# Performance work log

Measured on AMD Instinct MI355X. Metric: run time of the kernel, lower is better.

## Reference

```python
import jax, jax.numpy as jnp
import numpy as np

B, N, D, DH = 8, 2048, 1024, 64

def setup_inputs() -> dict:
    key = jax.random.key(0)
    ks = jax.random.split(key, 4)
    s = 1.0 / np.sqrt(D)
    return {
        "x": jax.random.normal(ks[0], (B, N, D), dtype=jnp.float32),
        "Wq": jax.random.normal(ks[1], (D, DH), dtype=jnp.float32) * s,
        "bq": jnp.zeros((DH,), dtype=jnp.float32),
        "Wk": jax.random.normal(ks[2], (D, DH), dtype=jnp.float32) * s,
        "bk": jnp.zeros((DH,), dtype=jnp.float32),
        "Wv": jax.random.normal(ks[3], (D, DH), dtype=jnp.float32) * s,
        "bv": jnp.zeros((DH,), dtype=jnp.float32),
    }

def reference(x, Wq, bq, Wk, bk, Wv, bv):
    # Projections: [B,N,DH]
    Q = x @ Wq + bq
    K = x @ Wk + bk
    V = x @ Wv + bv
    sqrt_dh = jnp.sqrt(jnp.asarray(DH, dtype=x.dtype))
    # scores[b,i,j] = Q_i . K_j  (original materializes [B,N,N,DH]; GEMM is equivalent math)
    att = jnp.einsum("bid,bjd->bij", Q, K) / sqrt_dh
    # NOTE: original softmaxes over dim=1 (the query/i axis), not the usual j axis.
    att = jax.nn.softmax(att, axis=1)
    # Dropout is identity in eval mode.
    return jnp.einsum("bij,bjd->bid", att, V)
```

## Files before the change

kernel.cpp:

```cpp
#include <hip/hip_runtime.h>
#include <math.h>

#define Bn  8
#define Nn  2048
#define Dn  1024
#define DHn 64
#define PAD 72

typedef __attribute__((ext_vector_type(8))) short bf16x8;
typedef __attribute__((ext_vector_type(4))) float f32x4;

static __device__ inline short f2bf(float f) {
    unsigned u = __builtin_bit_cast(unsigned, f);
    u += 0x7FFFu + ((u >> 16) & 1u);
    return (short)(u >> 16);
}
static __device__ inline bf16x8 pack8(float4 a, float4 b) {
    bf16x8 v;
    v[0] = f2bf(a.x); v[1] = f2bf(a.y); v[2] = f2bf(a.z); v[3] = f2bf(a.w);
    v[4] = f2bf(b.x); v[5] = f2bf(b.y); v[6] = f2bf(b.z); v[7] = f2bf(b.w);
    return v;
}

__global__ __launch_bounds__(128) void wt_kernel(
    const float* __restrict__ Wq, const float* __restrict__ Wk,
    const float* __restrict__ Wv, short* __restrict__ Wtf)
{
    const int nt = blockIdx.x / 16, kt = blockIdx.x % 16;
    const int t = threadIdx.x;
    const int half = t >> 6, l = t & 63;
    const int c = l & 15, quad = l >> 4;
    const int mat = nt >> 2, cm = (nt & 3) * 16 + c;
    const float* Wm = (mat == 0) ? Wq : (mat == 1 ? Wk : Wv);
    short* o = &Wtf[((((size_t)nt * 16 + kt) * 2 + half) * 64 + l) * 8];
#pragma unroll
    for (int e = 0; e < 8; ++e) {
        const int k = kt * 64 + half * 32 + quad * 8 + e;
        o[e] = f2bf(Wm[(size_t)k * DHn + cm]);
    }
}

__global__ __launch_bounds__(256) void qkv_kernel(
    const float* __restrict__ x, const short* __restrict__ Wtf,
    const float* __restrict__ bq, const float* __restrict__ bk,
    const float* __restrict__ bv,
    short* __restrict__ Qb, short* __restrict__ Kb, short* __restrict__ Vt)
{
    __shared__ __attribute__((aligned(16))) short xs[2][32][PAD];

    const int t = threadIdx.x;
    const int w = t >> 6, l = t & 63;
    const int c = l & 15, quad = l >> 4;
    const int ibase = blockIdx.x * 32;
    const int r0 = t >> 3, kc = t & 7;

    const float* xrow = &x[(size_t)(ibase + r0) * Dn + kc * 8];

    {
        const float4 a = ((const float4*)xrow)[0];
        const float4 b = ((const float4*)xrow)[1];
        *(bf16x8*)&xs[0][r0][kc * 8] = pack8(a, b);
    }

    f32x4 acc[2][3];
#pragma unroll
    for (int mt = 0; mt < 2; ++mt)
#pragma unroll
        for (int nt = 0; nt < 3; ++nt) acc[mt][nt] = (f32x4){0.f, 0.f, 0.f, 0.f};

    __syncthreads();

    for (int kt = 0; kt < 16; ++kt) {
        const int cur = kt & 1;
        float4 pa, pb;
        if (kt < 15) {
            pa = ((const float4*)(xrow + (kt + 1) * 64))[0];
            pb = ((const float4*)(xrow + (kt + 1) * 64))[1];
        }
#pragma unroll
        for (int h = 0; h < 2; ++h) {
            const bf16x8 af0 = *(const bf16x8*)&xs[cur][c][h * 32 + quad * 8];
            const bf16x8 af1 = *(const bf16x8*)&xs[cur][16 + c][h * 32 + quad * 8];
#pragma unroll
            for (int nt = 0; nt < 3; ++nt) {
                const int ntg = w * 3 + nt;
                const bf16x8 bf = *(const bf16x8*)&Wtf[((((size_t)ntg * 16 + kt) * 2 + h) * 64 + l) * 8];
                acc[0][nt] = __builtin_amdgcn_mfma_f32_16x16x32_bf16(af0, bf, acc[0][nt], 0, 0, 0);
                acc[1][nt] = __builtin_amdgcn_mfma_f32_16x16x32_bf16(af1, bf, acc[1][nt], 0, 0, 0);
            }
        }
        if (kt < 15) *(bf16x8*)&xs[1 - cur][r0][kc * 8] = pack8(pa, pb);
        __syncthreads();
    }

#pragma unroll
    for (int nt = 0; nt < 3; ++nt) {
        const int col = w * 48 + nt * 16 + c;
        const int mat = col >> 6, cm = col & 63;
        const float bias = (mat == 0 ? bq : (mat == 1 ? bk : bv))[cm];
#pragma unroll
        for (int mt = 0; mt < 2; ++mt) {
            if (mat == 2) {
                const int row = ibase + mt * 16 + quad * 4;
                const int b = row >> 11, i = row & (Nn - 1);
                ushort4 o;
                o.x = (unsigned short)f2bf(acc[mt][nt][0] + bias);
                o.y = (unsigned short)f2bf(acc[mt][nt][1] + bias);
                o.z = (unsigned short)f2bf(acc[mt][nt][2] + bias);
                o.w = (unsigned short)f2bf(acc[mt][nt][3] + bias);
                *(ushort4*)&Vt[((size_t)b * DHn + cm) * Nn + i] = o;
            } else {
                const float s = (mat == 1) ? 0.125f : 1.0f;
                short* Out = (mat == 0) ? Qb : Kb;
#pragma unroll
                for (int r = 0; r < 4; ++r)
                    Out[(size_t)(ibase + mt * 16 + quad * 4 + r) * DHn + cm] =
                        f2bf((acc[mt][nt][r] + bias) * s);
            }
        }
    }
}

__global__ __launch_bounds__(256) void colsum_kernel(
    const short* __restrict__ Qb, const short* __restrict__ Kb,
    float* __restrict__ lpart)
{
    __shared__ __attribute__((aligned(16))) short Qw[4][2][16][PAD];
    __shared__ float red[16][64];

    const int t = threadIdx.x;
    const int w = t >> 6, l = t & 63;
    const int c = l & 15, quad = l >> 4;
    const int bid = blockIdx.x;
    const int b = bid >> 7, rem = bid & 127, jt = rem >> 2, s = rem & 3;
    const int jbase = jt * 64;
    const int srow = l >> 2, scol = (l & 3) * 16;

    bf16x8 kb[4][2];
#pragma unroll
    for (int nt = 0; nt < 4; ++nt)
#pragma unroll
        for (int kk = 0; kk < 2; ++kk)
            kb[nt][kk] = *(const bf16x8*)&Kb[((size_t)b * Nn + jbase + nt * 16 + c) * DHn
                                             + kk * 32 + quad * 8];

    const short* qbase = &Qb[((size_t)b * Nn + s * 512 + w * 16 + srow) * DHn + scol];

    *(bf16x8*)&Qw[w][0][srow][scol]     = *(const bf16x8*)qbase;
    *(bf16x8*)&Qw[w][0][srow][scol + 8] = *(const bf16x8*)(qbase + 8);

    float lsum[4] = {0.f, 0.f, 0.f, 0.f};

    for (int ch = 0; ch < 8; ++ch) {
        const int cur = ch & 1;
        bf16x8 p0, p1;
        if (ch < 7) {
            const short* pq = qbase + (size_t)(ch + 1) * 64 * DHn;
            p0 = *(const bf16x8*)pq; p1 = *(const bf16x8*)(pq + 8);
        }
        const bf16x8 aq0 = *(const bf16x8*)&Qw[w][cur][c][quad * 8];
        const bf16x8 aq1 = *(const bf16x8*)&Qw[w][cur][c][32 + quad * 8];
#pragma unroll
        for (int nt = 0; nt < 4; ++nt) {
            f32x4 sv = (f32x4){0.f, 0.f, 0.f, 0.f};
            sv = __builtin_amdgcn_mfma_f32_16x16x32_bf16(aq0, kb[nt][0], sv, 0, 0, 0);
            sv = __builtin_amdgcn_mfma_f32_16x16x32_bf16(aq1, kb[nt][1], sv, 0, 0, 0);
            lsum[nt] += __expf(sv[0]) + __expf(sv[1]) + __expf(sv[2]) + __expf(sv[3]);
        }
        if (ch < 7) {
            *(bf16x8*)&Qw[w][1 - cur][srow][scol]     = p0;
            *(bf16x8*)&Qw[w][1 - cur][srow][scol + 8] = p1;
        }
    }

#pragma unroll
    for (int nt = 0; nt < 4; ++nt) red[w * 4 + quad][nt * 16 + c] = lsum[nt];
    __syncthreads();
    if (t < 64) {
        float sum = 0.f;
#pragma unroll
        for (int r = 0; r < 16; ++r) sum += red[r][t];
        lpart[((size_t)s * Bn + b) * Nn + jbase + t] = sum;
    }
}

__global__ __launch_bounds__(256) void attnout_kernel(
    const short* __restrict__ Qb, const short* __restrict__ Kb,
    const short* __restrict__ Vt, const float* __restrict__ lpart,
    float* __restrict__ outp)
{
    __shared__ __attribute__((aligned(16))) short Ks[2][64][PAD];
    __shared__ __attribute__((aligned(16))) short Vs[2][64][PAD];
    __shared__ __attribute__((aligned(16))) short Ps[4][16][PAD];
    __shared__ float rls[2][64];

    const int t = threadIdx.x;
    const int w = t >> 6, lane = t & 63;
    const int c = lane & 15, quad = lane >> 4;
    const int bid = blockIdx.x;
    const int b = bid >> 7, rem = bid & 127, it = rem >> 2, s = rem & 3;
    const int ibase = it * 64;
    const int r0 = t >> 2, cc = (t & 3) * 16;

    const size_t qrow = (size_t)b * Nn + ibase + w * 16 + c;
    const bf16x8 aq0 = *(const bf16x8*)&Qb[qrow * DHn + quad * 8];
    const bf16x8 aq1 = *(const bf16x8*)&Qb[qrow * DHn + 32 + quad * 8];

    const short* kbase = &Kb[((size_t)b * Nn + s * 512 + r0) * DHn + cc];
    const short* vbase = &Vt[((size_t)b * DHn + r0) * Nn + s * 512 + cc];

    *(bf16x8*)&Ks[0][r0][cc]     = *(const bf16x8*)kbase;
    *(bf16x8*)&Ks[0][r0][cc + 8] = *(const bf16x8*)(kbase + 8);
    *(bf16x8*)&Vs[0][r0][cc]     = *(const bf16x8*)vbase;
    *(bf16x8*)&Vs[0][r0][cc + 8] = *(const bf16x8*)(vbase + 8);
    if (t < 64) {
        const size_t lj = (size_t)b * Nn + s * 512 + t;
        rls[0][t] = 1.0f / (lpart[lj] + lpart[(size_t)Bn * Nn + lj]
                          + lpart[2 * (size_t)Bn * Nn + lj] + lpart[3 * (size_t)Bn * Nn + lj]);
    }

    f32x4 acc[4];
#pragma unroll
    for (int dn = 0; dn < 4; ++dn) acc[dn] = (f32x4){0.f, 0.f, 0.f, 0.f};
    __syncthreads();

    for (int jt2 = 0; jt2 < 8; ++jt2) {
        const int cur = jt2 & 1;
        bf16x8 pk0, pk1, pv0, pv1; float nrl;
        if (jt2 < 7) {
            const short* pk = kbase + (size_t)(jt2 + 1) * 64 * DHn;
            pk0 = *(const bf16x8*)pk; pk1 = *(const bf16x8*)(pk + 8);
            const short* pv = vbase + (jt2 + 1) * 64;
            pv0 = *(const bf16x8*)pv; pv1 = *(const bf16x8*)(pv + 8);
            if (t < 64) {
                const size_t lj = (size_t)b * Nn + s * 512 + (jt2 + 1) * 64 + t;
                nrl = 1.0f / (lpart[lj] + lpart[(size_t)Bn * Nn + lj]
                            + lpart[2 * (size_t)Bn * Nn + lj] + lpart[3 * (size_t)Bn * Nn + lj]);
            }
        }

#pragma unroll
        for (int nt = 0; nt < 4; ++nt) {
            const bf16x8 kb0 = *(const bf16x8*)&Ks[cur][nt * 16 + c][quad * 8];
            const bf16x8 kb1 = *(const bf16x8*)&Ks[cur][nt * 16 + c][32 + quad * 8];
            f32x4 sv = (f32x4){0.f, 0.f, 0.f, 0.f};
            sv = __builtin_amdgcn_mfma_f32_16x16x32_bf16(aq0, kb0, sv, 0, 0, 0);
            sv = __builtin_amdgcn_mfma_f32_16x16x32_bf16(aq1, kb1, sv, 0, 0, 0);
            const float rl = rls[cur][nt * 16 + c];
#pragma unroll
            for (int r = 0; r < 4; ++r)
                Ps[w][quad * 4 + r][nt * 16 + c] = f2bf(__expf(sv[r]) * rl);
        }
        const bf16x8 ap0 = *(const bf16x8*)&Ps[w][c][quad * 8];
        const bf16x8 ap1 = *(const bf16x8*)&Ps[w][c][32 + quad * 8];
#pragma unroll
        for (int dn = 0; dn < 4; ++dn) {
            const bf16x8 vb0 = *(const bf16x8*)&Vs[cur][dn * 16 + c][quad * 8];
            const bf16x8 vb1 = *(const bf16x8*)&Vs[cur][dn * 16 + c][32 + quad * 8];
            acc[dn] = __builtin_amdgcn_mfma_f32_16x16x32_bf16(ap0, vb0, acc[dn], 0, 0, 0);
            acc[dn] = __builtin_amdgcn_mfma_f32_16x16x32_bf16(ap1, vb1, acc[dn], 0, 0, 0);
        }

        if (jt2 < 7) {
            *(bf16x8*)&Ks[1 - cur][r0][cc]     = pk0;
            *(bf16x8*)&Ks[1 - cur][r0][cc + 8] = pk1;
            *(bf16x8*)&Vs[1 - cur][r0][cc]     = pv0;
            *(bf16x8*)&Vs[1 - cur][r0][cc + 8] = pv1;
            if (t < 64) rls[1 - cur][t] = nrl;
        }
        __syncthreads();
    }

    float* op = outp + (size_t)s * (Bn * Nn * DHn) + ((size_t)b * Nn + ibase) * DHn;
#pragma unroll
    for (int dn = 0; dn < 4; ++dn)
#pragma unroll
        for (int r = 0; r < 4; ++r)
            op[(w * 16 + quad * 4 + r) * DHn + dn * 16 + c] = acc[dn][r];
}

__global__ __launch_bounds__(256) void outreduce_kernel(
    const float* __restrict__ outp, float* __restrict__ out)
{
    const int id = blockIdx.x * 256 + threadIdx.x;
    const float4* p = (const float4*)outp;
    const float4 a = p[id];
    const float4 b = p[id + 262144];
    const float4 c = p[id + 2 * 262144];
    const float4 d = p[id + 3 * 262144];
    float4 r;
    r.x = a.x + b.x + c.x + d.x;
    r.y = a.y + b.y + c.y + d.y;
    r.z = a.z + b.z + c.z + d.z;
    r.w = a.w + b.w + c.w + d.w;
    ((float4*)out)[id] = r;
}

extern "C" void kernel_launch(void* const* d_in, const int* in_sizes, int n_in,
                              void* d_out, int out_size, void* d_ws, size_t ws_size,
                              hipStream_t stream)
{
    const float* x  = (const float*)d_in[0];
    const float* Wq = (const float*)d_in[1];
    const float* bq = (const float*)d_in[2];
    const float* Wk = (const float*)d_in[3];
    const float* bk = (const float*)d_in[4];
    const float* Wv = (const float*)d_in[5];
    const float* bv = (const float*)d_in[6];
    float* out = (float*)d_out;

    char* ws = (char*)d_ws;
    short* Qb    = (short*)(ws);
    short* Kb    = (short*)(ws + (size_t)(1 << 21));
    short* Vt    = (short*)(ws + (size_t)(2 << 21));
    short* Wtf   = (short*)(ws + (size_t)(3 << 21));
    float* lpart = (float*)(ws + (size_t)(3 << 21) + (1 << 19));
    float* outp  = (float*)(ws + (size_t)(7 << 20));

    wt_kernel<<<dim3(192), dim3(128), 0, stream>>>(Wq, Wk, Wv, Wtf);
    qkv_kernel<<<dim3(512), dim3(256), 0, stream>>>(x, Wtf, bq, bk, bv, Qb, Kb, Vt);
    colsum_kernel<<<dim3(1024), dim3(256), 0, stream>>>(Qb, Kb, lpart);
    attnout_kernel<<<dim3(1024), dim3(256), 0, stream>>>(Qb, Kb, Vt, lpart, outp);
    outreduce_kernel<<<dim3(1024), dim3(256), 0, stream>>>(outp, out);
}
```

Baseline: 160.3 us.

## Double query rows per wave in attention kernels and split keys eight ways

In attnout, each wave now handles 32 query rows (two 16-row subtiles), so every K/V tile loaded into shared memory feeds twice the MFMA work. The key dimension is split eight ways instead of four, which keeps the block count the same. In colsum, each wave processes 32 query rows per iteration with wider staging loads and half as many loop iterations. The cost is twice as many fp32 partial outputs written by attnout and read by outreduce, plus higher register use for the doubled accumulators. The workspace must also be large enough for eight partial buffers.

```diff
diff --git a/kernel.cpp b/kernel.cpp
--- a/kernel.cpp
+++ b/kernel.cpp
@@ -5,7 +5,8 @@
 #define Nn  2048
 #define Dn  1024
 #define DHn 64
-#define PAD 72
+#define PAD  72
+#define PADP 72
 
 typedef __attribute__((ext_vector_type(8))) short bf16x8;
 typedef __attribute__((ext_vector_type(4))) float f32x4;
@@ -125,7 +126,7 @@
     const short* __restrict__ Qb, const short* __restrict__ Kb,
     float* __restrict__ lpart)
 {
-    __shared__ __attribute__((aligned(16))) short Qw[4][2][16][PAD];
+    __shared__ __attribute__((aligned(16))) short Qw[4][2][32][PAD];
     __shared__ float red[16][64];
 
     const int t = threadIdx.x;
@@ -134,7 +135,7 @@
     const int bid = blockIdx.x;
     const int b = bid >> 7, rem = bid & 127, jt = rem >> 2, s = rem & 3;
     const int jbase = jt * 64;
-    const int srow = l >> 2, scol = (l & 3) * 16;
+    const int srow = l >> 1, scoff = (l & 1) * 32;
 
     bf16x8 kb[4][2];
 #pragma unroll
@@ -144,32 +145,38 @@
             kb[nt][kk] = *(const bf16x8*)&Kb[((size_t)b * Nn + jbase + nt * 16 + c) * DHn
                                              + kk * 32 + quad * 8];
 
-    const short* qbase = &Qb[((size_t)b * Nn + s * 512 + w * 16 + srow) * DHn + scol];
-
-    *(bf16x8*)&Qw[w][0][srow][scol]     = *(const bf16x8*)qbase;
-    *(bf16x8*)&Qw[w][0][srow][scol + 8] = *(const bf16x8*)(qbase + 8);
+    const short* qbase = &Qb[((size_t)b * Nn + s * 512 + w * 128 + srow) * DHn + scoff];
+
+#pragma unroll
+    for (int k = 0; k < 4; ++k)
+        *(bf16x8*)&Qw[w][0][srow][scoff + k * 8] = *(const bf16x8*)(qbase + k * 8);
 
     float lsum[4] = {0.f, 0.f, 0.f, 0.f};
 
-    for (int ch = 0; ch < 8; ++ch) {
-        const int cur = ch & 1;
-        bf16x8 p0, p1;
-        if (ch < 7) {
-            const short* pq = qbase + (size_t)(ch + 1) * 64 * DHn;
-            p0 = *(const bf16x8*)pq; p1 = *(const bf16x8*)(pq + 8);
-        }
-        const bf16x8 aq0 = *(const bf16x8*)&Qw[w][cur][c][quad * 8];
-        const bf16x8 aq1 = *(const bf16x8*)&Qw[w][cur][c][32 + quad * 8];
-#pragma unroll
-        for (int nt = 0; nt < 4; ++nt) {
-            f32x4 sv = (f32x4){0.f, 0.f, 0.f, 0.f};
-            sv = __builtin_amdgcn_mfma_f32_16x16x32_bf16(aq0, kb[nt][0], sv, 0, 0, 0);
-            sv = __builtin_amdgcn_mfma_f32_16x16x32_bf16(aq1, kb[nt][1], sv, 0, 0, 0);
-            lsum[nt] += __expf(sv[0]) + __expf(sv[1]) + __expf(sv[2]) + __expf(sv[3]);
-        }
-        if (ch < 7) {
-            *(bf16x8*)&Qw[w][1 - cur][srow][scol]     = p0;
-            *(bf16x8*)&Qw[w][1 - cur][srow][scol + 8] = p1;
+    for (int it2 = 0; it2 < 4; ++it2) {
+        const int cur = it2 & 1;
+        bf16x8 p[4];
+        if (it2 < 3) {
+            const short* pq = qbase + (size_t)(it2 + 1) * 32 * DHn;
+#pragma unroll
+            for (int k = 0; k < 4; ++k) p[k] = *(const bf16x8*)(pq + k * 8);
+        }
+#pragma unroll
+        for (int cc2 = 0; cc2 < 2; ++cc2) {
+            const bf16x8 aq0 = *(const bf16x8*)&Qw[w][cur][cc2 * 16 + c][quad * 8];
+            const bf16x8 aq1 = *(const bf16x8*)&Qw[w][cur][cc2 * 16 + c][32 + quad * 8];
+#pragma unroll
+            for (int nt = 0; nt < 4; ++nt) {
+                f32x4 sv = (f32x4){0.f, 0.f, 0.f, 0.f};
+                sv = __builtin_amdgcn_mfma_f32_16x16x32_bf16(aq0, kb[nt][0], sv, 0, 0, 0);
+                sv = __builtin_amdgcn_mfma_f32_16x16x32_bf16(aq1, kb[nt][1], sv, 0, 0, 0);
+                lsum[nt] += __expf(sv[0]) + __expf(sv[1]) + __expf(sv[2]) + __expf(sv[3]);
+            }
+        }
+        if (it2 < 3) {
+#pragma unroll
+            for (int k = 0; k < 4; ++k)
+                *(bf16x8*)&Qw[w][1 - cur][srow][scoff + k * 8] = p[k];
         }
     }
 
@@ -191,49 +198,55 @@
 {
     __shared__ __attribute__((aligned(16))) short Ks[2][64][PAD];
     __shared__ __attribute__((aligned(16))) short Vs[2][64][PAD];
-    __shared__ __attribute__((aligned(16))) short Ps[4][16][PAD];
+    __shared__ __attribute__((aligned(16))) short Ps[4][32][PADP];
     __shared__ float rls[2][64];
 
     const int t = threadIdx.x;
     const int w = t >> 6, lane = t & 63;
     const int c = lane & 15, quad = lane >> 4;
     const int bid = blockIdx.x;
-    const int b = bid >> 7, rem = bid & 127, it = rem >> 2, s = rem & 3;
-    const int ibase = it * 64;
+    const int b = bid >> 7, rem = bid & 127, it = rem >> 3, s = rem & 7;
+    const int ibase = it * 128;
     const int r0 = t >> 2, cc = (t & 3) * 16;
 
-    const size_t qrow = (size_t)b * Nn + ibase + w * 16 + c;
-    const bf16x8 aq0 = *(const bf16x8*)&Qb[qrow * DHn + quad * 8];
-    const bf16x8 aq1 = *(const bf16x8*)&Qb[qrow * DHn + 32 + quad * 8];
-
-    const short* kbase = &Kb[((size_t)b * Nn + s * 512 + r0) * DHn + cc];
-    const short* vbase = &Vt[((size_t)b * DHn + r0) * Nn + s * 512 + cc];
+    bf16x8 aq[2][2];
+#pragma unroll
+    for (int sub = 0; sub < 2; ++sub) {
+        const size_t qrow = (size_t)b * Nn + ibase + w * 32 + sub * 16 + c;
+        aq[sub][0] = *(const bf16x8*)&Qb[qrow * DHn + quad * 8];
+        aq[sub][1] = *(const bf16x8*)&Qb[qrow * DHn + 32 + quad * 8];
+    }
+
+    const short* kbase = &Kb[((size_t)b * Nn + s * 256 + r0) * DHn + cc];
+    const short* vbase = &Vt[((size_t)b * DHn + r0) * Nn + s * 256 + cc];
 
     *(bf16x8*)&Ks[0][r0][cc]     = *(const bf16x8*)kbase;
     *(bf16x8*)&Ks[0][r0][cc + 8] = *(const bf16x8*)(kbase + 8);
     *(bf16x8*)&Vs[0][r0][cc]     = *(const bf16x8*)vbase;
     *(bf16x8*)&Vs[0][r0][cc + 8] = *(const bf16x8*)(vbase + 8);
     if (t < 64) {
-        const size_t lj = (size_t)b * Nn + s * 512 + t;
+        const size_t lj = (size_t)b * Nn + s * 256 + t;
         rls[0][t] = 1.0f / (lpart[lj] + lpart[(size_t)Bn * Nn + lj]
                           + lpart[2 * (size_t)Bn * Nn + lj] + lpart[3 * (size_t)Bn * Nn + lj]);
     }
 
-    f32x4 acc[4];
-#pragma unroll
-    for (int dn = 0; dn < 4; ++dn) acc[dn] = (f32x4){0.f, 0.f, 0.f, 0.f};
+    f32x4 acc[2][4];
+#pragma unroll
+    for (int sub = 0; sub < 2; ++sub)
+#pragma unroll
+        for (int dn = 0; dn < 4; ++dn) acc[sub][dn] = (f32x4){0.f, 0.f, 0.f, 0.f};
     __syncthreads();
 
-    for (int jt2 = 0; jt2 < 8; ++jt2) {
+    for (int jt2 = 0; jt2 < 4; ++jt2) {
         const int cur = jt2 & 1;
         bf16x8 pk0, pk1, pv0, pv1; float nrl;
-        if (jt2 < 7) {
+        if (jt2 < 3) {
             const short* pk = kbase + (size_t)(jt2 + 1) * 64 * DHn;
             pk0 = *(const bf16x8*)pk; pk1 = *(const bf16x8*)(pk + 8);
             const short* pv = vbase + (jt2 + 1) * 64;
             pv0 = *(const bf16x8*)pv; pv1 = *(const bf16x8*)(pv + 8);
             if (t < 64) {
-                const size_t lj = (size_t)b * Nn + s * 512 + (jt2 + 1) * 64 + t;
+                const size_t lj = (size_t)b * Nn + s * 256 + (jt2 + 1) * 64 + t;
                 nrl = 1.0f / (lpart[lj] + lpart[(size_t)Bn * Nn + lj]
                             + lpart[2 * (size_t)Bn * Nn + lj] + lpart[3 * (size_t)Bn * Nn + lj]);
             }
@@ -243,25 +256,35 @@
         for (int nt = 0; nt < 4; ++nt) {
             const bf16x8 kb0 = *(const bf16x8*)&Ks[cur][nt * 16 + c][quad * 8];
             const bf16x8 kb1 = *(const bf16x8*)&Ks[cur][nt * 16 + c][32 + quad * 8];
-            f32x4 sv = (f32x4){0.f, 0.f, 0.f, 0.f};
-            sv = __builtin_amdgcn_mfma_f32_16x16x32_bf16(aq0, kb0, sv, 0, 0, 0);
-            sv = __builtin_amdgcn_mfma_f32_16x16x32_bf16(aq1, kb1, sv, 0, 0, 0);
             const float rl = rls[cur][nt * 16 + c];
 #pragma unroll
-            for (int r = 0; r < 4; ++r)
-                Ps[w][quad * 4 + r][nt * 16 + c] = f2bf(__expf(sv[r]) * rl);
-        }
-        const bf16x8 ap0 = *(const bf16x8*)&Ps[w][c][quad * 8];
-        const bf16x8 ap1 = *(const bf16x8*)&Ps[w][c][32 + quad * 8];
+            for (int sub = 0; sub < 2; ++sub) {
+                f32x4 sv = (f32x4){0.f, 0.f, 0.f, 0.f};
+                sv = __builtin_amdgcn_mfma_f32_16x16x32_bf16(aq[sub][0], kb0, sv, 0, 0, 0);
+                sv = __builtin_amdgcn_mfma_f32_16x16x32_bf16(aq[sub][1], kb1, sv, 0, 0, 0);
+#pragma unroll
+                for (int r = 0; r < 4; ++r)
+                    Ps[w][sub * 16 + quad * 4 + r][nt * 16 + c] = f2bf(__expf(sv[r]) * rl);
+            }
+        }
+        bf16x8 ap[2][2];
+#pragma unroll
+        for (int sub = 0; sub < 2; ++sub) {
+            ap[sub][0] = *(const bf16x8*)&Ps[w][sub * 16 + c][quad * 8];
+            ap[sub][1] = *(const bf16x8*)&Ps[w][sub * 16 + c][32 + quad * 8];
+        }
 #pragma unroll
         for (int dn = 0; dn < 4; ++dn) {
             const bf16x8 vb0 = *(const bf16x8*)&Vs[cur][dn * 16 + c][quad * 8];
             const bf16x8 vb1 = *(const bf16x8*)&Vs[cur][dn * 16 + c][32 + quad * 8];
-            acc[dn] = __builtin_amdgcn_mfma_f32_16x16x32_bf16(ap0, vb0, acc[dn], 0, 0, 0);
-            acc[dn] = __builtin_amdgcn_mfma_f32_16x16x32_bf16(ap1, vb1, acc[dn], 0, 0, 0);
-        }
-
-        if (jt2 < 7) {
+#pragma unroll
+            for (int sub = 0; sub < 2; ++sub) {
+                acc[sub][dn] = __builtin_amdgcn_mfma_f32_16x16x32_bf16(ap[sub][0], vb0, acc[sub][dn], 0, 0, 0);
+                acc[sub][dn] = __builtin_amdgcn_mfma_f32_16x16x32_bf16(ap[sub][1], vb1, acc[sub][dn], 0, 0, 0);
+            }
+        }
+
+        if (jt2 < 3) {
             *(bf16x8*)&Ks[1 - cur][r0][cc]     = pk0;
             *(bf16x8*)&Ks[1 - cur][r0][cc + 8] = pk1;
             *(bf16x8*)&Vs[1 - cur][r0][cc]     = pv0;
@@ -273,10 +296,12 @@
 
     float* op = outp + (size_t)s * (Bn * Nn * DHn) + ((size_t)b * Nn + ibase) * DHn;
 #pragma unroll
-    for (int dn = 0; dn < 4; ++dn)
-#pragma unroll
-        for (int r = 0; r < 4; ++r)
-            op[(w * 16 + quad * 4 + r) * DHn + dn * 16 + c] = acc[dn][r];
+    for (int sub = 0; sub < 2; ++sub)
+#pragma unroll
+        for (int dn = 0; dn < 4; ++dn)
+#pragma unroll
+            for (int r = 0; r < 4; ++r)
+                op[(w * 32 + sub * 16 + quad * 4 + r) * DHn + dn * 16 + c] = acc[sub][dn][r];
 }
 
 __global__ __launch_bounds__(256) void outreduce_kernel(
@@ -284,15 +309,12 @@
 {
     const int id = blockIdx.x * 256 + threadIdx.x;
     const float4* p = (const float4*)outp;
-    const float4 a = p[id];
-    const float4 b = p[id + 262144];
-    const float4 c = p[id + 2 * 262144];
-    const float4 d = p[id + 3 * 262144];
-    float4 r;
-    r.x = a.x + b.x + c.x + d.x;
-    r.y = a.y + b.y + c.y + d.y;
-    r.z = a.z + b.z + c.z + d.z;
-    r.w = a.w + b.w + c.w + d.w;
+    float4 r = p[id];
+#pragma unroll
+    for (int k = 1; k < 8; ++k) {
+        const float4 a = p[id + (size_t)k * 262144];
+        r.x += a.x; r.y += a.y; r.z += a.z; r.w += a.w;
+    }
     ((float4*)out)[id] = r;
 }
 
```

Result: no change. 157.4 us (-1.8%).

## Materialize exp scores in colsum, fold column normalization into V, drop QK recompute

Applied to the files above, without the earlier changes.

The column-sum kernel now also writes the bf16 exp(QK) tiles to a workspace buffer, already laid out in MFMA operand order. A new kernel divides V by the column sums, so the output kernel only streams the stored exp tiles and multiplies them by the scaled V, with no QK recompute or exp. This removes half of the MFMA work and the transcendental work in the output stage. In exchange it writes and reads a 64 MB intermediate, adds a kernel launch, and changes rounding because V is normalized before the bf16 product.

```diff
diff --git a/kernel.cpp b/kernel.cpp
--- a/kernel.cpp
+++ b/kernel.cpp
@@ -5,7 +5,8 @@
 #define Nn  2048
 #define Dn  1024
 #define DHn 64
-#define PAD 72
+#define PAD  72
+#define PADP 72
 
 typedef __attribute__((ext_vector_type(8))) short bf16x8;
 typedef __attribute__((ext_vector_type(4))) float f32x4;
@@ -14,6 +15,10 @@
     unsigned u = __builtin_bit_cast(unsigned, f);
     u += 0x7FFFu + ((u >> 16) & 1u);
     return (short)(u >> 16);
+}
+static __device__ inline float bf2f(short s) {
+    unsigned u = ((unsigned)(unsigned short)s) << 16;
+    return __builtin_bit_cast(float, u);
 }
 static __device__ inline bf16x8 pack8(float4 a, float4 b) {
     bf16x8 v;
@@ -123,9 +128,10 @@
 
 __global__ __launch_bounds__(256) void colsum_kernel(
     const short* __restrict__ Qb, const short* __restrict__ Kb,
-    float* __restrict__ lpart)
-{
-    __shared__ __attribute__((aligned(16))) short Qw[4][2][16][PAD];
+    float* __restrict__ lpart, short* __restrict__ Eb)
+{
+    __shared__ __attribute__((aligned(16))) short Qw[4][2][32][PAD];
+    __shared__ __attribute__((aligned(16))) short Ps[4][16][PADP];
     __shared__ float red[16][64];
 
     const int t = threadIdx.x;
@@ -134,7 +140,7 @@
     const int bid = blockIdx.x;
     const int b = bid >> 7, rem = bid & 127, jt = rem >> 2, s = rem & 3;
     const int jbase = jt * 64;
-    const int srow = l >> 2, scol = (l & 3) * 16;
+    const int srow = l >> 1, scoff = (l & 1) * 32;
 
     bf16x8 kb[4][2];
 #pragma unroll
@@ -144,32 +150,49 @@
             kb[nt][kk] = *(const bf16x8*)&Kb[((size_t)b * Nn + jbase + nt * 16 + c) * DHn
                                              + kk * 32 + quad * 8];
 
-    const short* qbase = &Qb[((size_t)b * Nn + s * 512 + w * 16 + srow) * DHn + scol];
-
-    *(bf16x8*)&Qw[w][0][srow][scol]     = *(const bf16x8*)qbase;
-    *(bf16x8*)&Qw[w][0][srow][scol + 8] = *(const bf16x8*)(qbase + 8);
+    const short* qbase = &Qb[((size_t)b * Nn + s * 512 + w * 128 + srow) * DHn + scoff];
+
+#pragma unroll
+    for (int k = 0; k < 4; ++k)
+        *(bf16x8*)&Qw[w][0][srow][scoff + k * 8] = *(const bf16x8*)(qbase + k * 8);
 
     float lsum[4] = {0.f, 0.f, 0.f, 0.f};
 
-    for (int ch = 0; ch < 8; ++ch) {
-        const int cur = ch & 1;
-        bf16x8 p0, p1;
-        if (ch < 7) {
-            const short* pq = qbase + (size_t)(ch + 1) * 64 * DHn;
-            p0 = *(const bf16x8*)pq; p1 = *(const bf16x8*)(pq + 8);
-        }
-        const bf16x8 aq0 = *(const bf16x8*)&Qw[w][cur][c][quad * 8];
-        const bf16x8 aq1 = *(const bf16x8*)&Qw[w][cur][c][32 + quad * 8];
-#pragma unroll
-        for (int nt = 0; nt < 4; ++nt) {
-            f32x4 sv = (f32x4){0.f, 0.f, 0.f, 0.f};
-            sv = __builtin_amdgcn_mfma_f32_16x16x32_bf16(aq0, kb[nt][0], sv, 0, 0, 0);
-            sv = __builtin_amdgcn_mfma_f32_16x16x32_bf16(aq1, kb[nt][1], sv, 0, 0, 0);
-            lsum[nt] += __expf(sv[0]) + __expf(sv[1]) + __expf(sv[2]) + __expf(sv[3]);
-        }
-        if (ch < 7) {
-            *(bf16x8*)&Qw[w][1 - cur][srow][scol]     = p0;
-            *(bf16x8*)&Qw[w][1 - cur][srow][scol + 8] = p1;
+    for (int it2 = 0; it2 < 4; ++it2) {
+        const int cur = it2 & 1;
+        bf16x8 p[4];
+        if (it2 < 3) {
+            const short* pq = qbase + (size_t)(it2 + 1) * 32 * DHn;
+#pragma unroll
+            for (int k = 0; k < 4; ++k) p[k] = *(const bf16x8*)(pq + k * 8);
+        }
+#pragma unroll
+        for (int cc2 = 0; cc2 < 2; ++cc2) {
+            const bf16x8 aq0 = *(const bf16x8*)&Qw[w][cur][cc2 * 16 + c][quad * 8];
+            const bf16x8 aq1 = *(const bf16x8*)&Qw[w][cur][cc2 * 16 + c][32 + quad * 8];
+#pragma unroll
+            for (int nt = 0; nt < 4; ++nt) {
+                f32x4 sv = (f32x4){0.f, 0.f, 0.f, 0.f};
+                sv = __builtin_amdgcn_mfma_f32_16x16x32_bf16(aq0, kb[nt][0], sv, 0, 0, 0);
+                sv = __builtin_amdgcn_mfma_f32_16x16x32_bf16(aq1, kb[nt][1], sv, 0, 0, 0);
+#pragma unroll
+                for (int r = 0; r < 4; ++r) {
+                    const float e = __expf(sv[r]);
+                    lsum[nt] += e;
+                    Ps[w][quad * 4 + r][nt * 16 + c] = f2bf(e);
+                }
+            }
+            const int f = s * 32 + w * 8 + it2 * 2 + cc2;
+            const bf16x8 ap0 = *(const bf16x8*)&Ps[w][c][quad * 8];
+            const bf16x8 ap1 = *(const bf16x8*)&Ps[w][c][32 + quad * 8];
+            short* eb = &Eb[((((size_t)b * 128 + f) * 64) + jt * 2) * 512 + l * 8];
+            *(bf16x8*)eb         = ap0;
+            *(bf16x8*)(eb + 512) = ap1;
+        }
+        if (it2 < 3) {
+#pragma unroll
+            for (int k = 0; k < 4; ++k)
+                *(bf16x8*)&Qw[w][1 - cur][srow][scoff + k * 8] = p[k];
         }
     }
 
@@ -184,89 +207,79 @@
     }
 }
 
+__global__ __launch_bounds__(256) void lscale_kernel(
+    short* __restrict__ Vt, const float* __restrict__ lpart)
+{
+    const int row = blockIdx.x;
+    const int b = row >> 6;
+    const int t = threadIdx.x;
+    const int j0 = t * 8;
+    bf16x8 v = *(const bf16x8*)&Vt[(size_t)row * Nn + j0];
+    float lv[8];
+#pragma unroll
+    for (int e = 0; e < 8; ++e) lv[e] = 0.f;
+#pragma unroll
+    for (int s = 0; s < 4; ++s) {
+        const float* lp = &lpart[((size_t)s * Bn + b) * Nn + j0];
+        const float4 a = ((const float4*)lp)[0];
+        const float4 bb = ((const float4*)lp)[1];
+        lv[0] += a.x;  lv[1] += a.y;  lv[2] += a.z;  lv[3] += a.w;
+        lv[4] += bb.x; lv[5] += bb.y; lv[6] += bb.z; lv[7] += bb.w;
+    }
+    bf16x8 o;
+#pragma unroll
+    for (int e = 0; e < 8; ++e) o[e] = f2bf(bf2f(v[e]) / lv[e]);
+    *(bf16x8*)&Vt[(size_t)row * Nn + j0] = o;
+}
+
 __global__ __launch_bounds__(256) void attnout_kernel(
-    const short* __restrict__ Qb, const short* __restrict__ Kb,
-    const short* __restrict__ Vt, const float* __restrict__ lpart,
+    const short* __restrict__ Eb, const short* __restrict__ Vt,
     float* __restrict__ outp)
 {
-    __shared__ __attribute__((aligned(16))) short Ks[2][64][PAD];
     __shared__ __attribute__((aligned(16))) short Vs[2][64][PAD];
-    __shared__ __attribute__((aligned(16))) short Ps[4][16][PAD];
-    __shared__ float rls[2][64];
-
-    const int t = threadIdx.x;
-    const int w = t >> 6, lane = t & 63;
-    const int c = lane & 15, quad = lane >> 4;
+
+    const int t = threadIdx.x;
+    const int w = t >> 6, l = t & 63;
+    const int c = l & 15, quad = l >> 4;
     const int bid = blockIdx.x;
     const int b = bid >> 7, rem = bid & 127, it = rem >> 2, s = rem & 3;
     const int ibase = it * 64;
+    const int f = it * 4 + w;
     const int r0 = t >> 2, cc = (t & 3) * 16;
 
-    const size_t qrow = (size_t)b * Nn + ibase + w * 16 + c;
-    const bf16x8 aq0 = *(const bf16x8*)&Qb[qrow * DHn + quad * 8];
-    const bf16x8 aq1 = *(const bf16x8*)&Qb[qrow * DHn + 32 + quad * 8];
-
-    const short* kbase = &Kb[((size_t)b * Nn + s * 512 + r0) * DHn + cc];
+    const short* ebase = &Eb[(((size_t)b * 128 + f) * 64 + s * 16) * 512 + l * 8];
     const short* vbase = &Vt[((size_t)b * DHn + r0) * Nn + s * 512 + cc];
 
-    *(bf16x8*)&Ks[0][r0][cc]     = *(const bf16x8*)kbase;
-    *(bf16x8*)&Ks[0][r0][cc + 8] = *(const bf16x8*)(kbase + 8);
     *(bf16x8*)&Vs[0][r0][cc]     = *(const bf16x8*)vbase;
     *(bf16x8*)&Vs[0][r0][cc + 8] = *(const bf16x8*)(vbase + 8);
-    if (t < 64) {
-        const size_t lj = (size_t)b * Nn + s * 512 + t;
-        rls[0][t] = 1.0f / (lpart[lj] + lpart[(size_t)Bn * Nn + lj]
-                          + lpart[2 * (size_t)Bn * Nn + lj] + lpart[3 * (size_t)Bn * Nn + lj]);
-    }
+    bf16x8 ea0 = *(const bf16x8*)(ebase);
+    bf16x8 ea1 = *(const bf16x8*)(ebase + 512);
 
     f32x4 acc[4];
 #pragma unroll
     for (int dn = 0; dn < 4; ++dn) acc[dn] = (f32x4){0.f, 0.f, 0.f, 0.f};
     __syncthreads();
 
-    for (int jt2 = 0; jt2 < 8; ++jt2) {
-        const int cur = jt2 & 1;
-        bf16x8 pk0, pk1, pv0, pv1; float nrl;
-        if (jt2 < 7) {
-            const short* pk = kbase + (size_t)(jt2 + 1) * 64 * DHn;
-            pk0 = *(const bf16x8*)pk; pk1 = *(const bf16x8*)(pk + 8);
-            const short* pv = vbase + (jt2 + 1) * 64;
+    for (int jj = 0; jj < 8; ++jj) {
+        const int cur = jj & 1;
+        bf16x8 pv0, pv1, pe0, pe1;
+        if (jj < 7) {
+            const short* pv = vbase + (jj + 1) * 64;
             pv0 = *(const bf16x8*)pv; pv1 = *(const bf16x8*)(pv + 8);
-            if (t < 64) {
-                const size_t lj = (size_t)b * Nn + s * 512 + (jt2 + 1) * 64 + t;
-                nrl = 1.0f / (lpart[lj] + lpart[(size_t)Bn * Nn + lj]
-                            + lpart[2 * (size_t)Bn * Nn + lj] + lpart[3 * (size_t)Bn * Nn + lj]);
-            }
-        }
-
-#pragma unroll
-        for (int nt = 0; nt < 4; ++nt) {
-            const bf16x8 kb0 = *(const bf16x8*)&Ks[cur][nt * 16 + c][quad * 8];
-            const bf16x8 kb1 = *(const bf16x8*)&Ks[cur][nt * 16 + c][32 + quad * 8];
-            f32x4 sv = (f32x4){0.f, 0.f, 0.f, 0.f};
-            sv = __builtin_amdgcn_mfma_f32_16x16x32_bf16(aq0, kb0, sv, 0, 0, 0);
-            sv = __builtin_amdgcn_mfma_f32_16x16x32_bf16(aq1, kb1, sv, 0, 0, 0);
-            const float rl = rls[cur][nt * 16 + c];
-#pragma unroll
-            for (int r = 0; r < 4; ++r)
-                Ps[w][quad * 4 + r][nt * 16 + c] = f2bf(__expf(sv[r]) * rl);
-        }
-        const bf16x8 ap0 = *(const bf16x8*)&Ps[w][c][quad * 8];
-        const bf16x8 ap1 = *(const bf16x8*)&Ps[w][c][32 + quad * 8];
+            pe0 = *(const bf16x8*)(ebase + (size_t)(jj * 2 + 2) * 512);
+            pe1 = *(const bf16x8*)(ebase + (size_t)(jj * 2 + 3) * 512);
+        }
 #pragma unroll
         for (int dn = 0; dn < 4; ++dn) {
             const bf16x8 vb0 = *(const bf16x8*)&Vs[cur][dn * 16 + c][quad * 8];
             const bf16x8 vb1 = *(const bf16x8*)&Vs[cur][dn * 16 + c][32 + quad * 8];
-            acc[dn] = __builtin_amdgcn_mfma_f32_16x16x32_bf16(ap0, vb0, acc[dn], 0, 0, 0);
-            acc[dn] = __builtin_amdgcn_mfma_f32_16x16x32_bf16(ap1, vb1, acc[dn], 0, 0, 0);
-        }
-
-        if (jt2 < 7) {
-            *(bf16x8*)&Ks[1 - cur][r0][cc]     = pk0;
-            *(bf16x8*)&Ks[1 - cur][r0][cc + 8] = pk1;
+            acc[dn] = __builtin_amdgcn_mfma_f32_16x16x32_bf16(ea0, vb0, acc[dn], 0, 0, 0);
+            acc[dn] = __builtin_amdgcn_mfma_f32_16x16x32_bf16(ea1, vb1, acc[dn], 0, 0, 0);
+        }
+        if (jj < 7) {
             *(bf16x8*)&Vs[1 - cur][r0][cc]     = pv0;
             *(bf16x8*)&Vs[1 - cur][r0][cc + 8] = pv1;
-            if (t < 64) rls[1 - cur][t] = nrl;
+            ea0 = pe0; ea1 = pe1;
         }
         __syncthreads();
     }
@@ -315,11 +328,13 @@
     short* Vt    = (short*)(ws + (size_t)(2 << 21));
     short* Wtf   = (short*)(ws + (size_t)(3 << 21));
     float* lpart = (float*)(ws + (size_t)(3 << 21) + (1 << 19));
-    float* outp  = (float*)(ws + (size_t)(7 << 20));
+    short* Eb    = (short*)(ws + (size_t)(8 << 20));
+    float* outp  = (float*)(ws + (size_t)(80 << 20));
 
     wt_kernel<<<dim3(192), dim3(128), 0, stream>>>(Wq, Wk, Wv, Wtf);
     qkv_kernel<<<dim3(512), dim3(256), 0, stream>>>(x, Wtf, bq, bk, bv, Qb, Kb, Vt);
-    colsum_kernel<<<dim3(1024), dim3(256), 0, stream>>>(Qb, Kb, lpart);
-    attnout_kernel<<<dim3(1024), dim3(256), 0, stream>>>(Qb, Kb, Vt, lpart, outp);
+    colsum_kernel<<<dim3(1024), dim3(256), 0, stream>>>(Qb, Kb, lpart, Eb);
+    lscale_kernel<<<dim3(512), dim3(256), 0, stream>>>(Vt, lpart);
+    attnout_kernel<<<dim3(1024), dim3(256), 0, stream>>>(Eb, Vt, outp);
     outreduce_kernel<<<dim3(1024), dim3(256), 0, stream>>>(outp, out);
 }
```

Result: no change. 162.0 us (+1.0%).
